# Optimization experiments

Hardware: AMD Instinct MI355X
Metric: run time of the kernel (lower is better)

Reference implementation:

```python
import jax, jax.numpy as jnp
import numpy as np

K = 7          # kernel_size (square)
P = K // 2     # padding
NUM_HEADS = 12


def setup_inputs() -> dict:
    key = jax.random.key(0)
    ks = jax.random.split(key, 6)
    B, H, W, D = 16, 56, 56, 768
    x = jax.random.normal(ks[0], (B, H, W, D), jnp.float32)
    qkv_w = jax.random.normal(ks[1], (3 * D, D), jnp.float32) * 0.02
    qkv_b = jnp.zeros((3 * D,), jnp.float32)
    rel_bias = jax.random.normal(ks[2], (1, NUM_HEADS, 1, K * K), jnp.float32)
    proj_w = jax.random.normal(ks[3], (D, D), jnp.float32) * 0.02
    proj_b = jnp.zeros((D,), jnp.float32)
    return {"x": x, "qkv_w": qkv_w, "qkv_b": qkv_b, "rel_bias": rel_bias,
            "proj_w": proj_w, "proj_b": proj_b}


def reference(x, qkv_w, qkv_b, rel_bias, proj_w, proj_b):
    B, H, W, D = x.shape
    hd = D // NUM_HEADS
    scale = 1.0 / np.sqrt(hd)

    qkv = x @ qkv_w.T + qkv_b                       # [B,H,W,3D]
    qkv = jnp.pad(qkv, ((0, 0), (P, P), (P, P), (0, 0)))  # zero-pad spatially
    Hp, Wp = H + 2 * P, W + 2 * P
    qkv = qkv.reshape(B, Hp, Wp, 3, NUM_HEADS, hd)
    qkv = jnp.transpose(qkv, (3, 0, 4, 1, 2, 5))    # [3,B,nh,Hp,Wp,hd]
    qf, kf, vf = qkv[0], qkv[1], qkv[2]

    q = qf[:, :, P:P + H, P:P + W, :]               # [B,nh,H,W,hd] (center pixel queries)

    # validity of each padded position (out-of-bounds keys get -inf, matching the torch mask)
    valid = jnp.pad(jnp.ones((H, W), dtype=bool), ((P, P), (P, P)))

    # scores per kernel offset; offsets iterate row-major (di, dj) matching
    # torch.meshgrid(..., indexing='ij') flattening used for relative_position_bias
    scores = []
    for di in range(K):
        for dj in range(K):
            ksh = kf[:, :, di:di + H, dj:dj + W, :]           # shifted keys [B,nh,H,W,hd]
            s = jnp.einsum('bnhwd,bnhwd->bnhw', q, ksh) * scale
            s = s + rel_bias[0, :, 0, di * K + dj][None, :, None, None]
            vmask = valid[di:di + H, dj:dj + W]
            s = jnp.where(vmask[None, None, :, :], s, -jnp.inf)
            scores.append(s)
    scores = jnp.stack(scores, axis=-1)             # [B,nh,H,W,K*K]
    attn = jax.nn.softmax(scores, axis=-1)

    out = jnp.zeros_like(q)
    for di in range(K):
        for dj in range(K):
            vsh = vf[:, :, di:di + H, dj:dj + W, :]
            out = out + attn[..., di * K + dj, None] * vsh

    out = jnp.transpose(out, (0, 2, 3, 1, 4)).reshape(B, H, W, D)
    return out @ proj_w.T + proj_b
```

## Files before the change

kernel.cpp:

```cpp
#include <hip/hip_runtime.h>
#include <hip/hip_bf16.h>

typedef __attribute__((ext_vector_type(8))) short short8;
typedef __attribute__((ext_vector_type(4))) short s16x4;
typedef __attribute__((ext_vector_type(4))) float f32x4;

#define AS1 __attribute__((address_space(1)))
#define AS3 __attribute__((address_space(3)))

__device__ __forceinline__ void gld16(const short* g, short* l) {
  __builtin_amdgcn_global_load_lds((const AS1 void*)g, (AS3 void*)l, 16, 0, 0);
}

__device__ __forceinline__ float bf2f(short x) {
  return __uint_as_float(((unsigned)(unsigned short)x) << 16);
}
__device__ __forceinline__ short f2bf(float f) {
  unsigned u = __float_as_uint(f);
  return (short)((u + 0x7fffu + ((u >> 16) & 1u)) >> 16);
}
__device__ __forceinline__ short f2bfn(float f) {
  __hip_bfloat16 h = __float2bfloat16(f);
  return *reinterpret_cast<short*>(&h);
}

#define XN8 4816896
#define QN8 221184
#define PN8 73728

__global__ void cast_all(const float* __restrict__ x, const float* __restrict__ qw,
                         const float* __restrict__ pw, short* __restrict__ xd,
                         short* __restrict__ qd, short* __restrict__ pd) {
  int stride = gridDim.x * blockDim.x;
  for (int i = blockIdx.x * blockDim.x + threadIdx.x;
       i < XN8 + QN8 + PN8; i += stride) {
    const float* s; short* d; int off;
    if (i < XN8)            { s = x;  d = xd; off = i; }
    else if (i < XN8 + QN8) { s = qw; d = qd; off = i - XN8; }
    else                    { s = pw; d = pd; off = i - (XN8 + QN8); }
    const float4* sp = (const float4*)(s + (size_t)off * 8);
    float4 a = sp[0], b = sp[1];
    short8 o;
    o[0] = f2bf(a.x); o[1] = f2bf(a.y); o[2] = f2bf(a.z); o[3] = f2bf(a.w);
    o[4] = f2bf(b.x); o[5] = f2bf(b.y); o[6] = f2bf(b.z); o[7] = f2bf(b.w);
    *(short8*)(d + (size_t)off * 8) = o;
  }
}

template<int OUT_BF16>
__global__ __launch_bounds__(256, 4) void gemm_bt(
    const short* __restrict__ A, const short* __restrict__ Bm,
    const float* __restrict__ bias, void* __restrict__ C,
    int M, int N, int Kd, int NB)
{
  __shared__ short As[128 * 64];
  __shared__ short Bs[128 * 64];
  const int tid = threadIdx.x;
  const int wave = tid >> 6, lane = tid & 63;

  int nwg = gridDim.x;
  int chunk = nwg >> 3;
  int bid = blockIdx.x;
  int nb2 = (bid & 7) * chunk + (bid >> 3);
  int per = NB << 3;
  int sr = nb2 / per, rem = nb2 - sr * per;
  int nblk = rem >> 3, mrow = rem & 7;
  int mblk = sr * 8 + mrow;

  size_t arow0 = (size_t)mblk * 128;
  size_t brow0 = (size_t)nblk * 128;
  const int wm = wave >> 1, wn = wave & 1;
  const int lr = lane & 15, grp = lane >> 4;

  const int swc = (tid & 7) ^ ((tid >> 3) & 7);
  const short* gA = A  + (arow0 + (tid >> 3)) * Kd + swc * 8;
  const short* gB = Bm + (brow0 + (tid >> 3)) * Kd + swc * 8;
  const size_t koA = (size_t)32 * Kd;
  short* ldsA = &As[wave * 512];
  short* ldsB = &Bs[wave * 512];

  f32x4 acc[4][4];
  #pragma unroll
  for (int i = 0; i < 4; ++i)
    #pragma unroll
    for (int j = 0; j < 4; ++j) {
      acc[i][j][0] = 0.f; acc[i][j][1] = 0.f; acc[i][j][2] = 0.f; acc[i][j][3] = 0.f;
    }

  int aoff[4][2], boff[4][2];
  #pragma unroll
  for (int mi = 0; mi < 4; ++mi) {
    int arow = wm * 64 + mi * 16 + lr;
    int brow = wn * 64 + mi * 16 + lr;
    #pragma unroll
    for (int kk = 0; kk < 2; ++kk) {
      int cb = (kk * 64 + grp * 16);
      aoff[mi][kk] = arow * 64 + ((cb ^ ((arow & 7) << 4)) >> 1);
      boff[mi][kk] = brow * 64 + ((cb ^ ((brow & 7) << 4)) >> 1);
    }
  }

  for (int k0 = 0; k0 < Kd; k0 += 64) {
    #pragma unroll
    for (int i = 0; i < 4; ++i) {
      gld16(gA + i * koA + k0, ldsA + i * 2048);
      gld16(gB + i * koA + k0, ldsB + i * 2048);
    }
    __syncthreads();
    #pragma unroll
    for (int kk = 0; kk < 2; ++kk) {
      short8 af[4], bfr[4];
      #pragma unroll
      for (int mi = 0; mi < 4; ++mi) {
        af[mi]  = *(const short8*)&As[aoff[mi][kk]];
        bfr[mi] = *(const short8*)&Bs[boff[mi][kk]];
      }
      #pragma unroll
      for (int i = 0; i < 4; ++i)
        #pragma unroll
        for (int j = 0; j < 4; ++j)
          acc[i][j] = __builtin_amdgcn_mfma_f32_16x16x32_bf16(af[i], bfr[j], acc[i][j], 0, 0, 0);
    }
    __syncthreads();
  }

  int r0 = grp * 4;
  #pragma unroll
  for (int i = 0; i < 4; ++i) {
    size_t grow0 = arow0 + wm * 64 + i * 16 + r0;
    #pragma unroll
    for (int j = 0; j < 4; ++j) {
      size_t gcol = brow0 + wn * 64 + j * 16 + lr;
      float bv = bias[gcol];
      #pragma unroll
      for (int r = 0; r < 4; ++r) {
        float v = acc[i][j][r] + bv;
        size_t off = (grow0 + r) * (size_t)N + gcol;
        if (OUT_BF16) ((short*)C)[off] = f2bf(v);
        else          ((float*)C)[off] = v;
      }
    }
  }
}

__global__ void build_idx(unsigned char* __restrict__ idxt) {
  int tile = blockIdx.x;
  int ht = tile >> 2, wt = tile & 3;
  int tid = threadIdx.x;
  int wave = tid >> 6, lane = tid & 63;
  int grp = lane >> 4, q = lane & 15;
  int Sw = (22 * wave) & ~7;
  unsigned w[12];
  #pragma unroll
  for (int i = 0; i < 12; ++i) w[i] = 0x31313131u;
  #pragma unroll
  for (int kt = 0; kt < 10; ++kt) {
    unsigned wd = 0;
    #pragma unroll
    for (int r = 0; r < 4; ++r) {
      int i22 = Sw + kt * 16 + grp * 4 + r;
      int hr = i22 / 22, hc = i22 - hr * 22;
      int dr = hr - wave, dc = hc - q;
      int kh = ht * 8 - 3 + hr, kw = wt * 16 - 3 + hc;
      bool valid = ((unsigned)dr < 7u) && ((unsigned)dc < 7u) &&
                   ((unsigned)kh < 56u) && ((unsigned)kw < 56u);
      unsigned o = valid ? (unsigned)(dr * 7 + dc) : 49u;
      wd |= o << (r * 8);
    }
    w[kt] = wd;
  }
  uint4* dst = (uint4*)(idxt + (((size_t)tile * 8 + wave) * 64 + lane) * 48);
  dst[0] = make_uint4(w[0], w[1], w[2], w[3]);
  dst[1] = make_uint4(w[4], w[5], w[6], w[7]);
  dst[2] = make_uint4(w[8], w[9], w[10], w[11]);
}

#define HALO_V 312
#define HVEC 308

__global__ __launch_bounds__(512, 4) void attn_mfma(
    const short* __restrict__ qkv, const float* __restrict__ rel_bias,
    const unsigned char* __restrict__ idxt, const short* __restrict__ zp,
    short* __restrict__ attn_out)
{
  __shared__ __align__(16) short kvbuf[HALO_V * 64];
  __shared__ float sbias[52];

  const int tid = threadIdx.x;
  const int wave = tid >> 6, lane = tid & 63;
  const int tile = blockIdx.x;
  const int ht = tile >> 2, wt = tile & 3;
  const int head = blockIdx.y % 12, b = blockIdx.y / 12;
  const int r0 = ht * 8, c0 = wt * 16;
  const int grp = lane >> 4, q = lane & 15;
  const int grp4 = grp * 4, grp8 = grp * 8;
  const int Sw = (22 * wave) & ~7;

  if (tid < 50)
    sbias[tid] = (tid < 49) ? rel_bias[head * 49 + tid] * 1.44269504f : -1e30f;

  const uint4* ip = (const uint4*)(idxt + (((size_t)tile * 8 + wave) * 64 + lane) * 48);
  uint4 iw0 = ip[0], iw1 = ip[1], iw2 = ip[2];
  unsigned idxw[10] = {iw0.x, iw0.y, iw0.z, iw0.w, iw1.x, iw1.y, iw1.z, iw1.w,
                       iw2.x, iw2.y};

  const int qrow = r0 + wave;
  const int qcol = min(c0 + q, 55);
  const short* qp = qkv + ((size_t)((b * 56 + qrow) * 56 + qcol)) * 2304 + head * 64;
  short8 qf0 = *(const short8*)(qp + grp8);
  short8 qf1 = *(const short8*)(qp + 32 + grp8);

  #pragma unroll
  for (int it = 0; it < 5; ++it) {
    int f = it * 512 + tid;
    if (f < HALO_V * 8) {
      int row = f >> 3, cc = f & 7;
      int hr = row / 22, hc = row - hr * 22;
      int gh = r0 - 3 + hr, gw = c0 - 3 + hc;
      bool ok = (row < HVEC) && ((unsigned)gh < 56u) && ((unsigned)gw < 56u);
      const short* src = ok
        ? qkv + ((size_t)((b * 56 + gh) * 56 + gw)) * 2304 + 768 + head * 64
              + ((cc ^ (row & 7)) * 8)
        : zp;
      gld16(src, &kvbuf[(it * 512 + wave * 64) * 8]);
    }
  }

  __syncthreads();

  short8 va[4], vb[4];
  int vq = 0, dcc = 0;
  const bool vact = (tid < HALO_V);
  if (vact) {
    vq = tid % 78; dcc = tid / 78;
    #pragma unroll
    for (int rr = 0; rr < 4; ++rr) {
      int vec = vq * 4 + rr;
      int hr = vec / 22, hc = vec - hr * 22;
      int gh = r0 - 3 + hr, gw = c0 - 3 + hc;
      bool ok = (vec < HVEC) && ((unsigned)gh < 56u) && ((unsigned)gw < 56u);
      const short8* vp = ok
        ? (const short8*)(qkv + ((size_t)((b * 56 + gh) * 56 + gw)) * 2304
                          + 1536 + head * 64 + dcc * 16)
        : (const short8*)zp;
      va[rr] = vp[0]; vb[rr] = vp[1];
    }
  }

  f32x4 accs[10];
  #pragma unroll
  for (int kt = 0; kt < 10; ++kt) {
    accs[kt][0] = 0.f; accs[kt][1] = 0.f; accs[kt][2] = 0.f; accs[kt][3] = 0.f;
  }
  __builtin_amdgcn_s_setprio(1);
  #pragma unroll
  for (int kt = 0; kt < 10; ++kt) {
    int vec = Sw + kt * 16 + q;
    int sw = vec & 7;
    short8 k0 = *(const short8*)&kvbuf[vec * 64 + ((grp ^ sw)) * 8];
    short8 k1 = *(const short8*)&kvbuf[vec * 64 + (((grp + 4) ^ sw)) * 8];
    accs[kt] = __builtin_amdgcn_mfma_f32_16x16x32_bf16(k0, qf0, accs[kt], 0, 0, 0);
    accs[kt] = __builtin_amdgcn_mfma_f32_16x16x32_bf16(k1, qf1, accs[kt], 0, 0, 0);
  }
  __builtin_amdgcn_s_setprio(0);

  __syncthreads();

  float sum = 0.f;
  unsigned plo[10], phi[10];
  #pragma unroll
  for (int kt = 0; kt < 10; ++kt) {
    float e[4];
    #pragma unroll
    for (int r = 0; r < 4; ++r) {
      float bia = sbias[(idxw[kt] >> (r * 8)) & 0xffu];
      float s = fmaf(accs[kt][r], 0.18033688f, bia);
      e[r] = __builtin_amdgcn_exp2f(s);
      sum += e[r];
    }
    plo[kt] = (unsigned)(unsigned short)f2bfn(e[0])
            | ((unsigned)(unsigned short)f2bfn(e[1]) << 16);
    phi[kt] = (unsigned)(unsigned short)f2bfn(e[2])
            | ((unsigned)(unsigned short)f2bfn(e[3]) << 16);
  }
  sum += __shfl_xor(sum, 16);
  sum += __shfl_xor(sum, 32);
  float inv = 1.0f / sum;

  if (vact) {
    #pragma unroll
    for (int dd = 0; dd < 8; ++dd) {
      s16x4 w;
      w[0] = va[0][dd]; w[1] = va[1][dd]; w[2] = va[2][dd]; w[3] = va[3][dd];
      *(s16x4*)&kvbuf[(dcc * 16 + dd) * HALO_V + vq * 4] = w;
    }
    #pragma unroll
    for (int dd = 0; dd < 8; ++dd) {
      s16x4 w;
      w[0] = vb[0][dd]; w[1] = vb[1][dd]; w[2] = vb[2][dd]; w[3] = vb[3][dd];
      *(s16x4*)&kvbuf[(dcc * 16 + 8 + dd) * HALO_V + vq * 4] = w;
    }
  }

  __syncthreads();

  const int src0 = ((grp & 1) << 5) + q;
  const bool hi = (grp >> 1) & 1;
  f32x4 acco[4];
  #pragma unroll
  for (int dt = 0; dt < 4; ++dt) {
    acco[dt][0] = 0.f; acco[dt][1] = 0.f; acco[dt][2] = 0.f; acco[dt][3] = 0.f;
  }
  #pragma unroll
  for (int km = 0; km < 5; ++km) {
    int aw0 = __shfl((int)plo[2*km], src0),      bw0 = __shfl((int)plo[2*km+1], src0);
    int aw1 = __shfl((int)phi[2*km], src0),      bw1 = __shfl((int)phi[2*km+1], src0);
    int aw2 = __shfl((int)plo[2*km], src0 + 16), bw2 = __shfl((int)plo[2*km+1], src0 + 16);
    int aw3 = __shfl((int)phi[2*km], src0 + 16), bw3 = __shfl((int)phi[2*km+1], src0 + 16);
    int4 wv = make_int4(hi ? bw0 : aw0, hi ? bw1 : aw1,
                        hi ? bw2 : aw2, hi ? bw3 : aw3);
    short8 pf = *(short8*)&wv;
    __builtin_amdgcn_s_setprio(1);
    #pragma unroll
    for (int dt = 0; dt < 4; ++dt) {
      short8 vf = *(const short8*)&kvbuf[(dt * 16 + q) * HALO_V + Sw + km * 32 + grp8];
      acco[dt] = __builtin_amdgcn_mfma_f32_16x16x32_bf16(pf, vf, acco[dt], 0, 0, 0);
    }
    __builtin_amdgcn_s_setprio(0);
  }

  float invr[4];
  #pragma unroll
  for (int r = 0; r < 4; ++r) invr[r] = __shfl(inv, grp4 + r);
  #pragma unroll
  for (int dt = 0; dt < 4; ++dt) {
    #pragma unroll
    for (int r = 0; r < 4; ++r) {
      int qc = c0 + grp4 + r;
      if (qc < 56) {
        size_t off = ((size_t)((b * 56 + qrow) * 56 + qc)) * 768
                     + head * 64 + dt * 16 + q;
        attn_out[off] = f2bfn(acco[dt][r] * invr[r]);
      }
    }
  }
}

extern "C" void kernel_launch(void* const* d_in, const int* in_sizes, int n_in,
                              void* d_out, int out_size, void* d_ws, size_t ws_size,
                              hipStream_t stream)
{
  const float* x      = (const float*)d_in[0];
  const float* qkv_w  = (const float*)d_in[1];
  const float* qkv_b  = (const float*)d_in[2];
  const float* rel_b  = (const float*)d_in[3];
  const float* proj_w = (const float*)d_in[4];
  const float* proj_b = (const float*)d_in[5];

  char* ws = (char*)d_ws;
  short* x_bf    = (short*)(ws);
  short* attn_bf = (short*)(ws);
  short* qw_bf   = (short*)(ws + 77070336);
  short* pw_bf   = (short*)(ws + 80609280);
  short* qkv_bf  = (short*)(ws + 81788928);
  unsigned char* idxt = (unsigned char*)(ws + 312999936);
  short* zp      = (short*)(ws + 313688064);

  hipMemsetAsync(zp, 0, 256, stream);
  build_idx<<<28, 512, 0, stream>>>(idxt);

  cast_all<<<2560, 256, 0, stream>>>(x, qkv_w, proj_w, x_bf, qw_bf, pw_bf);

  gemm_bt<1><<<392 * 18, 256, 0, stream>>>(x_bf, qw_bf, qkv_b, (void*)qkv_bf,
                                           50176, 2304, 768, 18);

  attn_mfma<<<dim3(28, 192), 512, 0, stream>>>(qkv_bf, rel_b, idxt, zp, attn_bf);

  gemm_bt<0><<<392 * 6, 256, 0, stream>>>(attn_bf, pw_bf, proj_b, d_out,
                                          50176, 768, 768, 6);
}
```

Before: 436.4 us.

## Replace 128x128 GEMM with 256x256 double-buffered, phase-pipelined MFMA GEMM

Both projection GEMMs now use a 512-thread 256x256 output tile with double-buffered LDS. Global-to-LDS loads for upcoming K-steps are interleaved with four MFMA phases separated by partial vmcnt waits and barriers, and s_setprio raises priority during the MFMA phases. The block-to-XCD remapping is generalized to handle grids that are not a multiple of 8. The goal is more reuse per loaded byte and overlap of memory with compute. In exchange it uses more LDS (128KB) and more accumulator registers, which lowers occupancy. The fine-grained vmcnt and barrier ordering is fragile.

New measurement: 441.2 us. Within noise of the previous version (+1.1%).

```diff
diff --git a/kernel.cpp b/kernel.cpp
--- a/kernel.cpp
+++ b/kernel.cpp
@@ -48,99 +48,196 @@
 }
 
 template<int OUT_BF16>
-__global__ __launch_bounds__(256, 4) void gemm_bt(
+__global__ __launch_bounds__(512, 2) void gemm256(
     const short* __restrict__ A, const short* __restrict__ Bm,
     const float* __restrict__ bias, void* __restrict__ C,
     int M, int N, int Kd, int NB)
 {
-  __shared__ short As[128 * 64];
-  __shared__ short Bs[128 * 64];
+  __shared__ short Asb[2][256 * 64];
+  __shared__ short Bsb[2][256 * 64];
   const int tid = threadIdx.x;
   const int wave = tid >> 6, lane = tid & 63;
 
   int nwg = gridDim.x;
-  int chunk = nwg >> 3;
-  int bid = blockIdx.x;
-  int nb2 = (bid & 7) * chunk + (bid >> 3);
-  int per = NB << 3;
+  int q8 = nwg >> 3, r8 = nwg & 7;
+  int xcd = blockIdx.x & 7, loc = blockIdx.x >> 3;
+  int nb2 = (xcd < r8 ? xcd * (q8 + 1) : r8 * (q8 + 1) + (xcd - r8) * q8) + loc;
+  int per = NB << 2;
   int sr = nb2 / per, rem = nb2 - sr * per;
-  int nblk = rem >> 3, mrow = rem & 7;
-  int mblk = sr * 8 + mrow;
-
-  size_t arow0 = (size_t)mblk * 128;
-  size_t brow0 = (size_t)nblk * 128;
-  const int wm = wave >> 1, wn = wave & 1;
+  int nblk = rem >> 2, mrow = rem & 3;
+  int mblk = sr * 4 + mrow;
+
+  size_t arow0 = (size_t)mblk * 256;
+  size_t brow0 = (size_t)nblk * 256;
+  const int wm = wave >> 2, wn = wave & 3;
   const int lr = lane & 15, grp = lane >> 4;
 
   const int swc = (tid & 7) ^ ((tid >> 3) & 7);
   const short* gA = A  + (arow0 + (tid >> 3)) * Kd + swc * 8;
   const short* gB = Bm + (brow0 + (tid >> 3)) * Kd + swc * 8;
-  const size_t koA = (size_t)32 * Kd;
-  short* ldsA = &As[wave * 512];
-  short* ldsB = &Bs[wave * 512];
-
-  f32x4 acc[4][4];
-  #pragma unroll
-  for (int i = 0; i < 4; ++i)
+  const size_t rs64 = (size_t)64 * Kd;
+  const int wb = wave * 512;
+
+  f32x4 acc[8][4];
+  #pragma unroll
+  for (int i = 0; i < 8; ++i)
     #pragma unroll
     for (int j = 0; j < 4; ++j) {
       acc[i][j][0] = 0.f; acc[i][j][1] = 0.f; acc[i][j][2] = 0.f; acc[i][j][3] = 0.f;
     }
 
-  int aoff[4][2], boff[4][2];
-  #pragma unroll
-  for (int mi = 0; mi < 4; ++mi) {
-    int arow = wm * 64 + mi * 16 + lr;
-    int brow = wn * 64 + mi * 16 + lr;
+  int aoff[8][2], boff[4][2];
+  #pragma unroll
+  for (int mi = 0; mi < 8; ++mi) {
+    int arow = mi * 32 + wm * 16 + lr;
     #pragma unroll
     for (int kk = 0; kk < 2; ++kk) {
-      int cb = (kk * 64 + grp * 16);
+      int cb = kk * 64 + grp * 16;
       aoff[mi][kk] = arow * 64 + ((cb ^ ((arow & 7) << 4)) >> 1);
-      boff[mi][kk] = brow * 64 + ((cb ^ ((brow & 7) << 4)) >> 1);
-    }
-  }
-
-  for (int k0 = 0; k0 < Kd; k0 += 64) {
-    #pragma unroll
-    for (int i = 0; i < 4; ++i) {
-      gld16(gA + i * koA + k0, ldsA + i * 2048);
-      gld16(gB + i * koA + k0, ldsB + i * 2048);
-    }
-    __syncthreads();
+    }
+  }
+  #pragma unroll
+  for (int nj = 0; nj < 4; ++nj) {
+    int brow = nj * 64 + wn * 16 + lr;
     #pragma unroll
     for (int kk = 0; kk < 2; ++kk) {
-      short8 af[4], bfr[4];
-      #pragma unroll
-      for (int mi = 0; mi < 4; ++mi) {
-        af[mi]  = *(const short8*)&As[aoff[mi][kk]];
-        bfr[mi] = *(const short8*)&Bs[boff[mi][kk]];
+      int cb = kk * 64 + grp * 16;
+      boff[nj][kk] = brow * 64 + ((cb ^ ((brow & 7) << 4)) >> 1);
+    }
+  }
+
+  const int NK = Kd >> 6;
+
+  auto stA = [&](int buf, int h, int koff) {
+    gld16(gA + (size_t)(h * 2) * rs64 + koff,     &Asb[buf][h * 8192 + wb]);
+    gld16(gA + (size_t)(h * 2 + 1) * rs64 + koff, &Asb[buf][h * 8192 + 4096 + wb]);
+  };
+  auto stB = [&](int buf, int h, int koff) {
+    gld16(gB + (size_t)(h * 2) * rs64 + koff,     &Bsb[buf][h * 8192 + wb]);
+    gld16(gB + (size_t)(h * 2 + 1) * rs64 + koff, &Bsb[buf][h * 8192 + 4096 + wb]);
+  };
+
+  stA(0, 0, 0); stB(0, 0, 0); stB(0, 1, 0); stA(0, 1, 0);
+  stA(1, 0, 64); stB(1, 0, 64); stB(1, 1, 64);
+  asm volatile("s_waitcnt vmcnt(6)" ::: "memory");
+  __builtin_amdgcn_s_barrier();
+  asm volatile("" ::: "memory");
+
+  short8 af[4][2], bA[2][2], bB[2][2];
+
+  #define PH_MFMA(MH, BF)                                                    \
+    __builtin_amdgcn_s_setprio(1);                                           \
+    _Pragma("unroll")                                                        \
+    for (int kk = 0; kk < 2; ++kk)                                           \
+      _Pragma("unroll")                                                      \
+      for (int r = 0; r < 2; ++r)                                            \
+        _Pragma("unroll")                                                    \
+        for (int mi = 0; mi < 4; ++mi)                                       \
+          acc[(MH)*4+mi][2*(BF)+r] = __builtin_amdgcn_mfma_f32_16x16x32_bf16(\
+              af[mi][kk], (BF ? bB : bA)[r][kk], acc[(MH)*4+mi][2*(BF)+r],   \
+              0, 0, 0);                                                      \
+    __builtin_amdgcn_s_setprio(0);
+
+  #define PH_SYNC()                                                          \
+    asm volatile("s_waitcnt vmcnt(8)" ::: "memory");                         \
+    __builtin_amdgcn_s_barrier();                                            \
+    asm volatile("" ::: "memory");
+
+  #define PH_END()                                                           \
+    asm volatile("" ::: "memory");                                           \
+    __builtin_amdgcn_s_barrier();                                            \
+    asm volatile("" ::: "memory");
+
+  for (int t = 0; t <= NK - 3; ++t) {
+    const short* pa = Asb[t & 1];
+    const short* pb = Bsb[t & 1];
+    const int k1 = (t + 1) << 6, k2 = (t + 2) << 6;
+
+    #pragma unroll
+    for (int mi = 0; mi < 4; ++mi)
+      #pragma unroll
+      for (int kk = 0; kk < 2; ++kk) af[mi][kk] = *(const short8*)&pa[aoff[mi][kk]];
+    #pragma unroll
+    for (int r = 0; r < 2; ++r)
+      #pragma unroll
+      for (int kk = 0; kk < 2; ++kk) bA[r][kk] = *(const short8*)&pb[boff[r][kk]];
+    stA((t + 1) & 1, 1, k1);
+    PH_SYNC();
+    PH_MFMA(0, 0);
+    PH_END();
+
+    #pragma unroll
+    for (int r = 0; r < 2; ++r)
+      #pragma unroll
+      for (int kk = 0; kk < 2; ++kk) bB[r][kk] = *(const short8*)&pb[boff[2 + r][kk]];
+    stA(t & 1, 0, k2);
+    PH_SYNC();
+    PH_MFMA(0, 1);
+    PH_END();
+
+    #pragma unroll
+    for (int mi = 0; mi < 4; ++mi)
+      #pragma unroll
+      for (int kk = 0; kk < 2; ++kk) af[mi][kk] = *(const short8*)&pa[aoff[4 + mi][kk]];
+    stB(t & 1, 0, k2);
+    PH_SYNC();
+    PH_MFMA(1, 0);
+    PH_END();
+
+    stB(t & 1, 1, k2);
+    PH_SYNC();
+    PH_MFMA(1, 1);
+    PH_END();
+  }
+
+  stA((NK - 1) & 1, 1, (NK - 1) << 6);
+  asm volatile("s_waitcnt vmcnt(0)" ::: "memory");
+  __builtin_amdgcn_s_barrier();
+  asm volatile("" ::: "memory");
+  #pragma unroll
+  for (int e = 0; e < 2; ++e) {
+    int tt = NK - 2 + e;
+    const short* pa = Asb[tt & 1];
+    const short* pb = Bsb[tt & 1];
+    #pragma unroll
+    for (int r = 0; r < 2; ++r)
+      #pragma unroll
+      for (int kk = 0; kk < 2; ++kk) {
+        bA[r][kk] = *(const short8*)&pb[boff[r][kk]];
+        bB[r][kk] = *(const short8*)&pb[boff[2 + r][kk]];
       }
-      #pragma unroll
-      for (int i = 0; i < 4; ++i)
+    #pragma unroll
+    for (int mh = 0; mh < 2; ++mh) {
+      #pragma unroll
+      for (int mi = 0; mi < 4; ++mi)
         #pragma unroll
-        for (int j = 0; j < 4; ++j)
-          acc[i][j] = __builtin_amdgcn_mfma_f32_16x16x32_bf16(af[i], bfr[j], acc[i][j], 0, 0, 0);
-    }
-    __syncthreads();
+        for (int kk = 0; kk < 2; ++kk)
+          af[mi][kk] = *(const short8*)&pa[aoff[mh * 4 + mi][kk]];
+      PH_MFMA(mh, 0);
+      PH_MFMA(mh, 1);
+    }
   }
 
   int r0 = grp * 4;
   #pragma unroll
-  for (int i = 0; i < 4; ++i) {
-    size_t grow0 = arow0 + wm * 64 + i * 16 + r0;
-    #pragma unroll
-    for (int j = 0; j < 4; ++j) {
-      size_t gcol = brow0 + wn * 64 + j * 16 + lr;
+  for (int mi = 0; mi < 8; ++mi) {
+    size_t grow0 = arow0 + mi * 32 + wm * 16 + r0;
+    #pragma unroll
+    for (int nj = 0; nj < 4; ++nj) {
+      size_t gcol = brow0 + nj * 64 + wn * 16 + lr;
       float bv = bias[gcol];
       #pragma unroll
       for (int r = 0; r < 4; ++r) {
-        float v = acc[i][j][r] + bv;
+        float v = acc[mi][nj][r] + bv;
         size_t off = (grow0 + r) * (size_t)N + gcol;
         if (OUT_BF16) ((short*)C)[off] = f2bf(v);
         else          ((float*)C)[off] = v;
       }
     }
   }
+  #undef PH_MFMA
+  #undef PH_SYNC
+  #undef PH_END
 }
 
 __global__ void build_idx(unsigned char* __restrict__ idxt) {
@@ -371,11 +468,11 @@
 
   cast_all<<<2560, 256, 0, stream>>>(x, qkv_w, proj_w, x_bf, qw_bf, pw_bf);
 
-  gemm_bt<1><<<392 * 18, 256, 0, stream>>>(x_bf, qw_bf, qkv_b, (void*)qkv_bf,
-                                           50176, 2304, 768, 18);
+  gemm256<1><<<1764, 512, 0, stream>>>(x_bf, qw_bf, qkv_b, (void*)qkv_bf,
+                                       50176, 2304, 768, 9);
 
   attn_mfma<<<dim3(28, 192), 512, 0, stream>>>(qkv_bf, rel_b, idxt, zp, attn_bf);
 
-  gemm_bt<0><<<392 * 6, 256, 0, stream>>>(attn_bf, pw_bf, proj_b, d_out,
-                                          50176, 768, 768, 6);
-}
+  gemm256<0><<<588, 512, 0, stream>>>(attn_bf, pw_bf, proj_b, d_out,
+                                      50176, 768, 768, 3);
+}
```
